# Performance work log

Hardware: AMD Instinct MI355X
Metric: run time of the kernel (lower is better)

## Reference

```python
import jax, jax.numpy as jnp
import numpy as np

NEG_INF = -9e15  # matches torch zero_vec constant
ALPHA = 0.2      # leaky relu slope


def setup_inputs() -> dict:
    key = jax.random.key(0)
    k1, k2, k3, k4, k5 = jax.random.split(key, 5)
    B, N, F_in, F_out = 8, 2048, 128, 64
    h = jax.random.normal(k1, (B, N, F_in), dtype=jnp.float32)
    adj = jax.random.randint(k2, (B, N, N), 0, 2, dtype=jnp.int32)
    # learned params: W (no bias), a = Linear(2*F_out, 1) split into a1, a2
    W = jax.random.normal(k3, (F_in, F_out), dtype=jnp.float32) / np.sqrt(F_in)
    a1 = jax.random.normal(k4, (F_out,), dtype=jnp.float32) / np.sqrt(2 * F_out)
    a2 = jax.random.normal(k5, (F_out,), dtype=jnp.float32) / np.sqrt(2 * F_out)
    return {"h": h, "adj": adj, "W": W, "a1": a1, "a2": a2}


def reference(h, adj, W, a1, a2):
    # Wh: (B, N, F_out)
    Wh = jnp.einsum('bnf,fo->bno', h, W)
    # a([Wh_i || Wh_j]) == a1·Wh_i + a2·Wh_j  (Linear has no bias)
    s1 = Wh @ a1  # (B, N) contribution of source node i
    s2 = Wh @ a2  # (B, N) contribution of target node j
    e = jax.nn.leaky_relu(s1[:, :, None] + s2[:, None, :], negative_slope=ALPHA)  # (B,N,N)
    scores = jnp.where(adj > 0, e, NEG_INF)
    attn = jax.nn.softmax(scores, axis=2)  # dropout inactive (eval mode)
    h_prime = jnp.einsum('bij,bjo->bio', attn, Wh)
    return jax.nn.elu(h_prime)
```

## Files before the change

### kernel.cpp

```cpp
#include <hip/hip_runtime.h>
#include <hip/hip_bf16.h>
#include <cmath>

#define NB 8
#define NN 2048
#define FIN 128
#define FOUT 64
#define GAT_ALPHA 0.2f

typedef __attribute__((ext_vector_type(8))) short short8;
typedef __attribute__((ext_vector_type(4))) float f32x4;

static __device__ __forceinline__ ushort f2bf(float x) {
    __hip_bfloat16 hb = __float2bfloat16(x);
    return __builtin_bit_cast(ushort, hb);
}

__global__ __launch_bounds__(256) void wh_kernel(const float* __restrict__ h,
                                                 const float* __restrict__ W,
                                                 const float* __restrict__ a1,
                                                 const float* __restrict__ a2,
                                                 ushort* __restrict__ whT,
                                                 float* __restrict__ s1,
                                                 float* __restrict__ s2) {
    __shared__ float tile[64][65];
    const int t = threadIdx.x;
    const int wave = t >> 6, lane = t & 63;
    const int b = blockIdx.x >> 5;
    const int j0 = (blockIdx.x & 31) << 6;
    const float a1v = a1[lane], a2v = a2[lane];

    for (int it = 0; it < 16; ++it) {
        const int jl = wave * 16 + it;
        const int row = b * NN + j0 + jl;
        const float4* h4 = (const float4*)(h + (size_t)row * FIN);
        float acc0 = 0.f, acc1 = 0.f, acc2 = 0.f, acc3 = 0.f;
#pragma unroll
        for (int f4 = 0; f4 < FIN / 4; ++f4) {
            const float4 hv = h4[f4];
            acc0 = fmaf(hv.x, W[(f4 * 4 + 0) * FOUT + lane], acc0);
            acc1 = fmaf(hv.y, W[(f4 * 4 + 1) * FOUT + lane], acc1);
            acc2 = fmaf(hv.z, W[(f4 * 4 + 2) * FOUT + lane], acc2);
            acc3 = fmaf(hv.w, W[(f4 * 4 + 3) * FOUT + lane], acc3);
        }
        const float acc = (acc0 + acc1) + (acc2 + acc3);
        tile[jl][lane] = acc;
        float r1 = acc * a1v, r2 = acc * a2v;
#pragma unroll
        for (int off = 32; off; off >>= 1) { r1 += __shfl_xor(r1, off); r2 += __shfl_xor(r2, off); }
        if (lane == 0) { s1[row] = r1; s2[row] = r2; }
    }
    __syncthreads();
#pragma unroll
    for (int rep = 0; rep < 16; ++rep) {
        const int o = rep * 4 + wave;
        whT[((size_t)(b * FOUT + o)) * NN + j0 + lane] = f2bf(tile[lane][o]);
    }
}

__global__ __launch_bounds__(256) void attn_kernel(const int* __restrict__ adj,
                                                   const ushort* __restrict__ whT,
                                                   const float* __restrict__ s1,
                                                   const float* __restrict__ s2,
                                                   float* __restrict__ out) {
    __shared__ float s2l[NN];
    __shared__ float red[4][16][FOUT];
    __shared__ float den[4][16];

    const int t = threadIdx.x, w = t >> 6, lane = t & 63;
    const int b = blockIdx.x >> 7;
    const int i0 = (blockIdx.x & 127) << 4;

    for (int idx = t; idx < NN; idx += 256) s2l[idx] = s2[b * NN + idx];

    const int rrow = lane & 15;
    const int kg   = lane >> 4;
    const float s1v = s1[b * NN + i0 + rrow];
    const int* adjRow = adj + ((size_t)(b * NN + i0 + rrow)) * NN;
    const ushort* whB = whT + (size_t)b * FOUT * NN;
    __syncthreads();

    f32x4 acc[4] = {{0.f,0.f,0.f,0.f},{0.f,0.f,0.f,0.f},{0.f,0.f,0.f,0.f},{0.f,0.f,0.f,0.f}};
    float dsum = 0.f;
    const int jbase = w * (NN / 4) + kg * 8;

    for (int step = 0; step < 16; ++step) {
        const int jb = jbase + step * 32;
        const int4 av0 = *(const int4*)(adjRow + jb);
        const int4 av1 = *(const int4*)(adjRow + jb + 4);
        const float4 sv0 = *(const float4*)(s2l + jb);
        const float4 sv1 = *(const float4*)(s2l + jb + 4);

        float p[8];
        {
            const int   a[8] = {av0.x, av0.y, av0.z, av0.w, av1.x, av1.y, av1.z, av1.w};
            const float s[8] = {sv0.x, sv0.y, sv0.z, sv0.w, sv1.x, sv1.y, sv1.z, sv1.w};
#pragma unroll
            for (int r = 0; r < 8; ++r) {
                const float x = s1v + s[r];
                const float e = x > 0.f ? x : GAT_ALPHA * x;
                p[r] = (a[r] > 0) ? __expf(e) : 0.f;
            }
        }
        dsum += ((p[0] + p[1]) + (p[2] + p[3])) + ((p[4] + p[5]) + (p[6] + p[7]));

        short8 af;
#pragma unroll
        for (int r = 0; r < 8; ++r) af[r] = (short)f2bf(p[r]);

#pragma unroll
        for (int nt = 0; nt < 4; ++nt) {
            const short8 bf = *(const short8*)(whB + ((size_t)(nt * 16 + rrow)) * NN + jb);
            acc[nt] = __builtin_amdgcn_mfma_f32_16x16x32_bf16(af, bf, acc[nt], 0, 0, 0);
        }
    }

    dsum += __shfl_xor(dsum, 16);
    dsum += __shfl_xor(dsum, 32);
    if (lane < 16) den[w][lane] = dsum;

#pragma unroll
    for (int nt = 0; nt < 4; ++nt)
#pragma unroll
        for (int q = 0; q < 4; ++q)
            red[w][kg * 4 + q][nt * 16 + rrow] = acc[nt][q];
    __syncthreads();

#pragma unroll
    for (int rep = 0; rep < 4; ++rep) {
        const int idx = rep * 256 + t;
        const int r = idx >> 6, o = idx & 63;
        const float num = red[0][r][o] + red[1][r][o] + red[2][r][o] + red[3][r][o];
        const float d = den[0][r] + den[1][r] + den[2][r] + den[3][r];
        const float v = num / d;
        out[((size_t)(b * NN + i0 + r)) * FOUT + o] = v > 0.f ? v : expm1f(v);
    }
}

extern "C" void kernel_launch(void* const* d_in, const int* in_sizes, int n_in,
                              void* d_out, int out_size, void* d_ws, size_t ws_size,
                              hipStream_t stream) {
    const float* h   = (const float*)d_in[0];
    const int*   adj = (const int*)d_in[1];
    const float* W   = (const float*)d_in[2];
    const float* a1  = (const float*)d_in[3];
    const float* a2  = (const float*)d_in[4];
    float* out = (float*)d_out;

    ushort* whT = (ushort*)d_ws;
    float*  s1  = (float*)((char*)d_ws + (size_t)NB * FOUT * NN * sizeof(ushort));
    float*  s2  = s1 + (size_t)NB * NN;

    wh_kernel<<<NB * 32, 256, 0, stream>>>(h, W, a1, a2, whT, s1, s2);
    attn_kernel<<<NB * 128, 256, 0, stream>>>(adj, whT, s1, s2, out);
}
```

Measured before the change: 275.5 us.

## Split attention over key halves, use MFMA for Wh projection, prefetch adjacency

The Wh projection now uses bf16 MFMA with a pre-transposed bf16 W from a new tiny kernel, and s1/s2 come from a folded W·a vector. The attention kernel splits each row block's key range into two halves, doubling the grid to 2048 blocks. It writes partial numerators and denominators, which a new reduce kernel combines before applying ELU. Adjacency loads are double-buffered in registers to hide global latency. The cost is extra launches, an extra partial-sum round-trip through memory, and lower precision for h in the projection.

```diff
diff --git a/kernel.cpp b/kernel.cpp
--- a/kernel.cpp
+++ b/kernel.cpp
@@ -15,46 +15,80 @@
     __hip_bfloat16 hb = __float2bfloat16(x);
     return __builtin_bit_cast(ushort, hb);
 }
+static __device__ __forceinline__ short8 pack8(const float4 a, const float4 b) {
+    short8 r;
+    r[0] = (short)f2bf(a.x); r[1] = (short)f2bf(a.y); r[2] = (short)f2bf(a.z); r[3] = (short)f2bf(a.w);
+    r[4] = (short)f2bf(b.x); r[5] = (short)f2bf(b.y); r[6] = (short)f2bf(b.z); r[7] = (short)f2bf(b.w);
+    return r;
+}
+
+__global__ void wt_kernel(const float* __restrict__ W, const float* __restrict__ a1,
+                          const float* __restrict__ a2, ushort* __restrict__ WT,
+                          float* __restrict__ wa) {
+    const int t = threadIdx.x;
+    const int o = t & 63, kg = t >> 6;
+#pragma unroll
+    for (int kk = 0; kk < 32; ++kk) {
+        const int k = kg * 32 + kk;
+        WT[o * FIN + k] = f2bf(W[k * FOUT + o]);
+    }
+    if (t < FIN) {
+        float x1 = 0.f, x2 = 0.f;
+        for (int o2 = 0; o2 < FOUT; ++o2) {
+            const float w = W[t * FOUT + o2];
+            x1 = fmaf(w, a1[o2], x1);
+            x2 = fmaf(w, a2[o2], x2);
+        }
+        wa[t] = x1; wa[FIN + t] = x2;
+    }
+}
 
 __global__ __launch_bounds__(256) void wh_kernel(const float* __restrict__ h,
-                                                 const float* __restrict__ W,
-                                                 const float* __restrict__ a1,
-                                                 const float* __restrict__ a2,
+                                                 const ushort* __restrict__ WT,
+                                                 const float* __restrict__ wa,
                                                  ushort* __restrict__ whT,
                                                  float* __restrict__ s1,
                                                  float* __restrict__ s2) {
-    __shared__ float tile[64][65];
-    const int t = threadIdx.x;
-    const int wave = t >> 6, lane = t & 63;
-    const int b = blockIdx.x >> 5;
-    const int j0 = (blockIdx.x & 31) << 6;
-    const float a1v = a1[lane], a2v = a2[lane];
-
-    for (int it = 0; it < 16; ++it) {
-        const int jl = wave * 16 + it;
-        const int row = b * NN + j0 + jl;
-        const float4* h4 = (const float4*)(h + (size_t)row * FIN);
-        float acc0 = 0.f, acc1 = 0.f, acc2 = 0.f, acc3 = 0.f;
-#pragma unroll
-        for (int f4 = 0; f4 < FIN / 4; ++f4) {
-            const float4 hv = h4[f4];
-            acc0 = fmaf(hv.x, W[(f4 * 4 + 0) * FOUT + lane], acc0);
-            acc1 = fmaf(hv.y, W[(f4 * 4 + 1) * FOUT + lane], acc1);
-            acc2 = fmaf(hv.z, W[(f4 * 4 + 2) * FOUT + lane], acc2);
-            acc3 = fmaf(hv.w, W[(f4 * 4 + 3) * FOUT + lane], acc3);
-        }
-        const float acc = (acc0 + acc1) + (acc2 + acc3);
-        tile[jl][lane] = acc;
-        float r1 = acc * a1v, r2 = acc * a2v;
-#pragma unroll
-        for (int off = 32; off; off >>= 1) { r1 += __shfl_xor(r1, off); r2 += __shfl_xor(r2, off); }
-        if (lane == 0) { s1[row] = r1; s2[row] = r2; }
-    }
-    __syncthreads();
-#pragma unroll
-    for (int rep = 0; rep < 16; ++rep) {
-        const int o = rep * 4 + wave;
-        whT[((size_t)(b * FOUT + o)) * NN + j0 + lane] = f2bf(tile[lane][o]);
+    const int t = threadIdx.x, w = t >> 6, lane = t & 63;
+    const int rrow = lane & 15, kg = lane >> 4;
+    const int j0 = blockIdx.x * 16;
+    const int b = j0 >> 11, jloc = j0 & (NN - 1);
+    const float* hrow = h + (size_t)(j0 + rrow) * FIN + kg * 8;
+
+    float4 hv[8];
+    short8 af[4];
+#pragma unroll
+    for (int ks = 0; ks < 4; ++ks) {
+        hv[2 * ks]     = *(const float4*)(hrow + ks * 32);
+        hv[2 * ks + 1] = *(const float4*)(hrow + ks * 32 + 4);
+        af[ks] = pack8(hv[2 * ks], hv[2 * ks + 1]);
+    }
+    f32x4 acc = {0.f, 0.f, 0.f, 0.f};
+#pragma unroll
+    for (int ks = 0; ks < 4; ++ks) {
+        const short8 bf = *(const short8*)(WT + (size_t)(w * 16 + rrow) * FIN + ks * 32 + kg * 8);
+        acc = __builtin_amdgcn_mfma_f32_16x16x32_bf16(af[ks], bf, acc, 0, 0, 0);
+    }
+#pragma unroll
+    for (int q = 0; q < 4; ++q)
+        whT[(((size_t)b * FOUT + w * 16 + rrow) << 11) + jloc + kg * 4 + q] = f2bf(acc[q]);
+
+    if (w == 0) {
+        float p1 = 0.f, p2 = 0.f;
+#pragma unroll
+        for (int ks = 0; ks < 4; ++ks) {
+#pragma unroll
+            for (int e = 0; e < 8; ++e) {
+                const float4 hq = hv[2 * ks + (e >> 2)];
+                const float x = (e & 3) == 0 ? hq.x : (e & 3) == 1 ? hq.y : (e & 3) == 2 ? hq.z : hq.w;
+                const int k = ks * 32 + kg * 8 + e;
+                p1 = fmaf(x, wa[k], p1);
+                p2 = fmaf(x, wa[FIN + k], p2);
+            }
+        }
+        p1 += __shfl_xor(p1, 16); p1 += __shfl_xor(p1, 32);
+        p2 += __shfl_xor(p2, 16); p2 += __shfl_xor(p2, 32);
+        if (lane < 16) { s1[j0 + lane] = p1; s2[j0 + lane] = p2; }
     }
 }
 
@@ -62,79 +96,95 @@
                                                    const ushort* __restrict__ whT,
                                                    const float* __restrict__ s1,
                                                    const float* __restrict__ s2,
-                                                   float* __restrict__ out) {
-    __shared__ float s2l[NN];
-    __shared__ float red[4][16][FOUT];
+                                                   float* __restrict__ pnum,
+                                                   float* __restrict__ pden) {
+    __shared__ float smem[4 * 16 * FOUT];
     __shared__ float den[4][16];
-
     const int t = threadIdx.x, w = t >> 6, lane = t & 63;
-    const int b = blockIdx.x >> 7;
-    const int i0 = (blockIdx.x & 127) << 4;
-
-    for (int idx = t; idx < NN; idx += 256) s2l[idx] = s2[b * NN + idx];
-
-    const int rrow = lane & 15;
-    const int kg   = lane >> 4;
+    const int rrow = lane & 15, kg = lane >> 4;
+    const int b = blockIdx.x >> 8, blk = blockIdx.x & 255;
+    const int i0 = (blk >> 1) << 4, half = blk & 1;
+    const int jh = half * (NN / 2);
+
+    for (int idx = t; idx < NN / 2; idx += 256) smem[idx] = s2[b * NN + jh + idx];
     const float s1v = s1[b * NN + i0 + rrow];
-    const int* adjRow = adj + ((size_t)(b * NN + i0 + rrow)) * NN;
-    const ushort* whB = whT + (size_t)b * FOUT * NN;
+    const int* adjRow = adj + ((size_t)(b * NN + i0 + rrow)) * NN + jh;
+    const ushort* whB = whT + (size_t)b * FOUT * NN + jh;
     __syncthreads();
 
-    f32x4 acc[4] = {{0.f,0.f,0.f,0.f},{0.f,0.f,0.f,0.f},{0.f,0.f,0.f,0.f},{0.f,0.f,0.f,0.f}};
+    f32x4 acc[4] = {{0,0,0,0},{0,0,0,0},{0,0,0,0},{0,0,0,0}};
     float dsum = 0.f;
-    const int jbase = w * (NN / 4) + kg * 8;
-
-    for (int step = 0; step < 16; ++step) {
-        const int jb = jbase + step * 32;
-        const int4 av0 = *(const int4*)(adjRow + jb);
-        const int4 av1 = *(const int4*)(adjRow + jb + 4);
-        const float4 sv0 = *(const float4*)(s2l + jb);
-        const float4 sv1 = *(const float4*)(s2l + jb + 4);
-
-        float p[8];
-        {
-            const int   a[8] = {av0.x, av0.y, av0.z, av0.w, av1.x, av1.y, av1.z, av1.w};
-            const float s[8] = {sv0.x, sv0.y, sv0.z, sv0.w, sv1.x, sv1.y, sv1.z, sv1.w};
-#pragma unroll
-            for (int r = 0; r < 8; ++r) {
-                const float x = s1v + s[r];
-                const float e = x > 0.f ? x : GAT_ALPHA * x;
-                p[r] = (a[r] > 0) ? __expf(e) : 0.f;
-            }
-        }
-        dsum += ((p[0] + p[1]) + (p[2] + p[3])) + ((p[4] + p[5]) + (p[6] + p[7]));
-
+    const int jb0 = w * 256 + kg * 8;
+
+    int4 buf[2][2];
+    buf[0][0] = *(const int4*)(adjRow + jb0);
+    buf[0][1] = *(const int4*)(adjRow + jb0 + 4);
+    buf[1][0] = *(const int4*)(adjRow + jb0 + 32);
+    buf[1][1] = *(const int4*)(adjRow + jb0 + 36);
+
+#pragma unroll
+    for (int step = 0; step < 8; ++step) {
+        const int jb = jb0 + step * 32;
+        const int4 c0 = buf[step & 1][0];
+        const int4 c1 = buf[step & 1][1];
+        if (step + 2 < 8) {
+            buf[step & 1][0] = *(const int4*)(adjRow + jb + 64);
+            buf[step & 1][1] = *(const int4*)(adjRow + jb + 68);
+        }
+        const float4 sv0 = *(const float4*)(smem + jb);
+        const float4 sv1 = *(const float4*)(smem + jb + 4);
+        const int   a[8] = {c0.x, c0.y, c0.z, c0.w, c1.x, c1.y, c1.z, c1.w};
+        const float s[8] = {sv0.x, sv0.y, sv0.z, sv0.w, sv1.x, sv1.y, sv1.z, sv1.w};
         short8 af;
-#pragma unroll
-        for (int r = 0; r < 8; ++r) af[r] = (short)f2bf(p[r]);
-
+        float ds = 0.f;
+#pragma unroll
+        for (int r = 0; r < 8; ++r) {
+            const float x = s1v + s[r];
+            const float e = __expf(fmaxf(x, GAT_ALPHA * x));
+            const float p = (a[r] > 0) ? e : 0.f;
+            ds += p;
+            af[r] = (short)f2bf(p);
+        }
+        dsum += ds;
 #pragma unroll
         for (int nt = 0; nt < 4; ++nt) {
-            const short8 bf = *(const short8*)(whB + ((size_t)(nt * 16 + rrow)) * NN + jb);
+            const short8 bf = *(const short8*)(whB + ((size_t)(nt * 16 + rrow) << 11) + jb);
             acc[nt] = __builtin_amdgcn_mfma_f32_16x16x32_bf16(af, bf, acc[nt], 0, 0, 0);
         }
     }
-
     dsum += __shfl_xor(dsum, 16);
     dsum += __shfl_xor(dsum, 32);
     if (lane < 16) den[w][lane] = dsum;
+    __syncthreads();
 
 #pragma unroll
     for (int nt = 0; nt < 4; ++nt)
 #pragma unroll
         for (int q = 0; q < 4; ++q)
-            red[w][kg * 4 + q][nt * 16 + rrow] = acc[nt][q];
+            smem[(w * 16 + kg * 4 + q) * FOUT + nt * 16 + rrow] = acc[nt][q];
     __syncthreads();
 
+    const size_t obase = (((size_t)half * NB + b) * NN + i0) * FOUT;
 #pragma unroll
     for (int rep = 0; rep < 4; ++rep) {
         const int idx = rep * 256 + t;
         const int r = idx >> 6, o = idx & 63;
-        const float num = red[0][r][o] + red[1][r][o] + red[2][r][o] + red[3][r][o];
-        const float d = den[0][r] + den[1][r] + den[2][r] + den[3][r];
-        const float v = num / d;
-        out[((size_t)(b * NN + i0 + r)) * FOUT + o] = v > 0.f ? v : expm1f(v);
-    }
+        pnum[obase + (size_t)r * FOUT + o] = smem[r * FOUT + o] + smem[(16 + r) * FOUT + o]
+                                          + smem[(32 + r) * FOUT + o] + smem[(48 + r) * FOUT + o];
+    }
+    if (t < 16) pden[((size_t)half * NB + b) * NN + i0 + t] =
+        den[0][t] + den[1][t] + den[2][t] + den[3][t];
+}
+
+__global__ __launch_bounds__(256) void reduce_kernel(const float* __restrict__ pnum,
+                                                     const float* __restrict__ pden,
+                                                     float* __restrict__ out) {
+    const int idx = blockIdx.x * 256 + threadIdx.x;
+    const int bi = idx >> 6;
+    const float num = pnum[idx] + pnum[idx + (size_t)NB * NN * FOUT];
+    const float d = pden[bi] + pden[bi + NB * NN];
+    const float v = num / d;
+    out[idx] = v > 0.f ? v : expm1f(v);
 }
 
 extern "C" void kernel_launch(void* const* d_in, const int* in_sizes, int n_in,
@@ -147,10 +197,17 @@
     const float* a2  = (const float*)d_in[4];
     float* out = (float*)d_out;
 
-    ushort* whT = (ushort*)d_ws;
-    float*  s1  = (float*)((char*)d_ws + (size_t)NB * FOUT * NN * sizeof(ushort));
-    float*  s2  = s1 + (size_t)NB * NN;
-
-    wh_kernel<<<NB * 32, 256, 0, stream>>>(h, W, a1, a2, whT, s1, s2);
-    attn_kernel<<<NB * 128, 256, 0, stream>>>(adj, whT, s1, s2, out);
-}
+    char* ws = (char*)d_ws;
+    ushort* whT = (ushort*)ws;  ws += (size_t)NB * FOUT * NN * sizeof(ushort);
+    ushort* WT  = (ushort*)ws;  ws += (size_t)FOUT * FIN * sizeof(ushort);
+    float*  wa  = (float*)ws;   ws += (size_t)2 * FIN * sizeof(float);
+    float*  s1  = (float*)ws;   ws += (size_t)NB * NN * sizeof(float);
+    float*  s2  = (float*)ws;   ws += (size_t)NB * NN * sizeof(float);
+    float*  pnum = (float*)ws;  ws += (size_t)2 * NB * NN * FOUT * sizeof(float);
+    float*  pden = (float*)ws;  ws += (size_t)2 * NB * NN * sizeof(float);
+
+    wt_kernel<<<1, 256, 0, stream>>>(W, a1, a2, WT, wa);
+    wh_kernel<<<NB * NN / 16, 256, 0, stream>>>(h, WT, wa, whT, s1, s2);
+    attn_kernel<<<NB * 256, 256, 0, stream>>>(adj, whT, s1, s2, pnum, pden);
+    reduce_kernel<<<NB * NN * FOUT / 256, 256, 0, stream>>>(pnum, pden, out);
+}
```

Result: faster. 237.1 us (-13.9%).
